# Kernel tuning notes

Measured on AMD Instinct MI355X. Metric: run time of the kernel, lower is better.

Reference implementation:

```python
import jax, jax.numpy as jnp
import numpy as np
from itertools import product

GRID = 64      # voxel grid resolution per scene
B = 8          # number of point clouds in the sparse batch
PER_B = 12500  # active voxels per scene
C = 64         # num_channels
K = 27         # 3x3x3 kernel offsets
EPS = 1e-5     # MinkowskiBatchNorm eps


def _build_kernel_map(coords):
    # coords: [N,4] int (b,x,y,z). For each of 27 offsets, find the input index
    # whose coordinate equals (b, x+dx, y+dy, z+dz); missing -> N (zero row).
    N = coords.shape[0]
    base = GRID + 2  # room for +-1 offsets after +1 shift

    def enc(b, x, y, z):
        return ((b.astype(np.int64) * base + (x + 1)) * base + (y + 1)) * base + (z + 1)

    keys = enc(coords[:, 0], coords[:, 1], coords[:, 2], coords[:, 3])
    order = np.argsort(keys)
    skeys = keys[order]
    kmap = np.full((N, K), N, dtype=np.int32)
    for k, (dx, dy, dz) in enumerate(product([-1, 0, 1], repeat=3)):
        qk = enc(coords[:, 0], coords[:, 1] + dx, coords[:, 2] + dy, coords[:, 3] + dz)
        pos = np.searchsorted(skeys, qk)
        posc = np.clip(pos, 0, N - 1)
        hit = skeys[posc] == qk
        kmap[:, k] = np.where(hit, order[posc], N)
    return kmap


def setup_inputs() -> dict:
    rng = np.random.default_rng(0)
    coords = []
    for b in range(B):
        flat = rng.choice(GRID ** 3, size=PER_B, replace=False)
        x = flat // (GRID * GRID)
        y = (flat // GRID) % GRID
        z = flat % GRID
        coords.append(np.stack([np.full(PER_B, b), x, y, z], axis=1))
    coords = np.concatenate(coords, axis=0)  # [N,4]
    kmap = _build_kernel_map(coords)         # [N,27]

    key = jax.random.key(0)
    k0, k1, k2 = jax.random.split(key, 3)
    N = coords.shape[0]
    x = jax.random.normal(k0, (N, C), dtype=jnp.float32)
    scale = 1.0 / np.sqrt(K * C)
    W1 = jax.random.normal(k1, (K, C, C), dtype=jnp.float32) * scale
    W2 = jax.random.normal(k2, (K, C, C), dtype=jnp.float32) * scale
    return {
        "x": x,
        "kmap": jnp.asarray(kmap),
        "gamma1": jnp.ones((C,), jnp.float32),
        "beta1": jnp.zeros((C,), jnp.float32),
        "W1": W1,
        "gamma2": jnp.ones((C,), jnp.float32),
        "beta2": jnp.zeros((C,), jnp.float32),
        "W2": W2,
    }


def _bn(h, gamma, beta):
    # MinkowskiBatchNorm (training mode): stats over all active points per channel
    m = h.mean(axis=0)
    v = h.var(axis=0)
    return (h - m) * jax.lax.rsqrt(v + EPS) * gamma + beta


def _sparse_conv(h, kmap, W):
    # MinkowskiConvolution stride=1: gather per-offset neighbors, GEMM, sum.
    hp = jnp.concatenate([h, jnp.zeros((1, h.shape[1]), h.dtype)], axis=0)  # zero row for misses
    g = hp[kmap]  # [N, K, C]
    return jnp.einsum('nkc,kcd->nd', g, W)


def reference(x, kmap, gamma1, beta1, W1, gamma2, beta2, W2):
    # pre-act: BN -> ReLU -> conv -> BN -> ReLU -> conv -> + residual
    out = _sparse_conv(jax.nn.relu(_bn(x, gamma1, beta1)), kmap, W1)
    out = _sparse_conv(jax.nn.relu(_bn(out, gamma2, beta2)), kmap, W2)
    return out + x
```

## Files before the change

kernel.cpp:

```cpp
#include <hip/hip_runtime.h>
#include <hip/hip_bf16.h>

#define CCH 64
#define KOFF 27
#define EPSV 1e-5f

typedef short bf16x8 __attribute__((ext_vector_type(8)));
typedef float f32x4  __attribute__((ext_vector_type(4)));

__device__ __forceinline__ void gld16(const void* g, void* l) {
    __builtin_amdgcn_global_load_lds((const __attribute__((address_space(1))) void*)g,
                                     (__attribute__((address_space(3))) void*)l, 16, 0, 0);
}

__global__ __launch_bounds__(256) void k_pre(const float* __restrict__ W1,
                                             const float* __restrict__ W2,
                                             __hip_bfloat16* __restrict__ img1,
                                             __hip_bfloat16* __restrict__ img2,
                                             const float* __restrict__ x, int N,
                                             float* __restrict__ sum,
                                             float* __restrict__ sumsq) {
    if (blockIdx.x < 2 * KOFF) {
        int k = blockIdx.x;
        const float* W = W1; __hip_bfloat16* img = img1;
        if (k >= KOFF) { k -= KOFF; W = W2; img = img2; }
        const float* src = W + (size_t)k * CCH * CCH;
        __hip_bfloat16* dst = img + (size_t)k * CCH * CCH;
        for (int e = threadIdx.x; e < CCH * CCH; e += 256) {
            const int p = e >> 3, j = e & 7;
            const int n = p >> 7, half = (p >> 6) & 1, chunk = (p >> 4) & 3, col = p & 15;
            dst[e] = __float2bfloat16(src[(chunk * 8 + half * 32 + j) * CCH + n * 16 + col]);
        }
        return;
    }
    const int bid = blockIdx.x - 2 * KOFF;
    const int nb  = gridDim.x - 2 * KOFF;
    const int c4  = threadIdx.x & 15;
    const int rg  = threadIdx.x >> 4;
    f32x4 s = {0.f, 0.f, 0.f, 0.f}, s2 = {0.f, 0.f, 0.f, 0.f};
    for (int r = bid * 16 + rg; r < N; r += nb * 16) {
        const float4 v = ((const float4*)x)[(size_t)r * 16 + c4];
        s[0] += v.x; s[1] += v.y; s[2] += v.z; s[3] += v.w;
        s2[0] += v.x * v.x; s2[1] += v.y * v.y; s2[2] += v.z * v.z; s2[3] += v.w * v.w;
    }
    __shared__ float sh[2][16][64];
#pragma unroll
    for (int j = 0; j < 4; ++j) {
        sh[0][rg][c4 * 4 + j] = s[j];
        sh[1][rg][c4 * 4 + j] = s2[j];
    }
    __syncthreads();
    if (threadIdx.x < 128) {
        const int which = threadIdx.x >> 6;
        const int c     = threadIdx.x & 63;
        float a = 0.f;
#pragma unroll
        for (int g = 0; g < 16; ++g) a += sh[which][g][c];
        atomicAdd(which ? &sumsq[c] : &sum[c], a);
    }
}

__global__ __launch_bounds__(256) void k_bnrelu_bf16(const float* __restrict__ x,
                                                     const float* __restrict__ sum,
                                                     const float* __restrict__ sumsq,
                                                     const float* __restrict__ gamma,
                                                     const float* __restrict__ beta,
                                                     __hip_bfloat16* __restrict__ h,
                                                     int N) {
    const float invN = 1.0f / (float)N;
    const int total = (N + 1) * 8;
    for (int i = blockIdx.x * 256 + threadIdx.x; i < total; i += gridDim.x * 256) {
        const int r  = i >> 3;
        const int c0 = (i & 7) * 8;
        union { __hip_bfloat16 b[8]; int4 v; } pk;
        if (r < N) {
            const float4 va = ((const float4*)x)[i * 2];
            const float4 vb = ((const float4*)x)[i * 2 + 1];
            const float vv[8] = {va.x, va.y, va.z, va.w, vb.x, vb.y, vb.z, vb.w};
#pragma unroll
            for (int j = 0; j < 8; ++j) {
                const int c     = c0 + j;
                const float m   = sum[c] * invN;
                const float var = sumsq[c] * invN - m * m;
                const float sc  = gamma[c] * rsqrtf(var + EPSV);
                const float sh_ = beta[c] - m * sc;
                float t = vv[j] * sc + sh_;
                t = t > 0.0f ? t : 0.0f;
                pk.b[j] = __float2bfloat16(t);
            }
        } else {
            pk.v = make_int4(0, 0, 0, 0);
        }
        ((int4*)h)[i] = pk.v;
    }
}

__global__ __launch_bounds__(256) void k_conv_mfma(const __hip_bfloat16* __restrict__ h,
                                                   const int* __restrict__ kmap,
                                                   const __hip_bfloat16* __restrict__ Wimg,
                                                   const float* __restrict__ resid,
                                                   float* __restrict__ out, int N,
                                                   float* __restrict__ stat_sum,
                                                   float* __restrict__ stat_sq) {
    __shared__ int sidx[64 * KOFF];
    __shared__ __hip_bfloat16 wbuf[2][4096];
    __shared__ float st[2][64];

    const int t     = threadIdx.x;
    const int lane  = t & 63;
    const int wave  = t >> 6;
    const int col16 = lane & 15;
    const int chunk = lane >> 4;
    const int base  = blockIdx.x * 64;
    const int p0    = base + wave * 16;

    const long gbase = (long)base * KOFF;
    const long glim  = (long)N * KOFF;
    for (int j = t; j < 64 * KOFF; j += 256)
        sidx[j] = (gbase + j < glim) ? kmap[gbase + j] : N;

    {
        const __hip_bfloat16* g = Wimg + t * 8;
        gld16(g,        &wbuf[0][t * 8]);
        gld16(g + 2048, &wbuf[0][t * 8 + 2048]);
    }
    __syncthreads();

    const int r0 = wave * 16 + col16;

    f32x4  acc[4] = {};
    bf16x8 a0p, a1p;

    {
        const int i0 = sidx[r0 * KOFF];
        const bf16x8* A0 = (const bf16x8*)(h + (size_t)i0 * CCH) + chunk;
        a0p = A0[0]; a1p = A0[4];
    }

    for (int k = 0; k < KOFF; ++k) {
        if (k + 1 < KOFF) {
            const __hip_bfloat16* g = Wimg + (size_t)(k + 1) * 4096 + t * 8;
            const int nb = (k + 1) & 1;
            gld16(g,        &wbuf[nb][t * 8]);
            gld16(g + 2048, &wbuf[nb][t * 8 + 2048]);
        }
        const bf16x8 a0 = a0p, a1 = a1p;
        if (k + 1 < KOFF) {
            const int i0 = sidx[r0 * KOFF + k + 1];
            const bf16x8* A0 = (const bf16x8*)(h + (size_t)i0 * CCH) + chunk;
            a0p = A0[0]; a1p = A0[4];
        }
        const bf16x8* bp = (const bf16x8*)&wbuf[k & 1][0] + lane;
#pragma unroll
        for (int n = 0; n < 4; ++n) {
            const bf16x8 b0 = bp[(n * 2 + 0) * 64];
            const bf16x8 b1 = bp[(n * 2 + 1) * 64];
            acc[n] = __builtin_amdgcn_mfma_f32_16x16x32_bf16(a0, b0, acc[n], 0, 0, 0);
            acc[n] = __builtin_amdgcn_mfma_f32_16x16x32_bf16(a1, b1, acc[n], 0, 0, 0);
        }
        __syncthreads();
    }

    if (stat_sum && t < 128) st[t >> 6][t & 63] = 0.0f;
    if (stat_sum) __syncthreads();

#pragma unroll
    for (int n = 0; n < 4; ++n) {
        const int col = n * 16 + col16;
        float s = 0.f, s2 = 0.f;
#pragma unroll
        for (int j = 0; j < 4; ++j) {
            const int row = p0 + chunk * 4 + j;
            if (row < N) {
                float v = acc[n][j];
                if (resid) v += resid[(size_t)row * CCH + col];
                out[(size_t)row * CCH + col] = v;
                s += v; s2 += v * v;
            }
        }
        if (stat_sum) {
            atomicAdd(&st[0][col], s);
            atomicAdd(&st[1][col], s2);
        }
    }
    if (stat_sum) {
        __syncthreads();
        if (t < 64)       atomicAdd(&stat_sum[t], st[0][t]);
        else if (t < 128) atomicAdd(&stat_sq[t - 64], st[1][t - 64]);
    }
}

extern "C" void kernel_launch(void* const* d_in, const int* in_sizes, int n_in,
                              void* d_out, int out_size, void* d_ws, size_t ws_size,
                              hipStream_t stream) {
    const float* x      = (const float*)d_in[0];
    const int*   kmap   = (const int*)d_in[1];
    const float* gamma1 = (const float*)d_in[2];
    const float* beta1  = (const float*)d_in[3];
    const float* W1     = (const float*)d_in[4];
    const float* gamma2 = (const float*)d_in[5];
    const float* beta2  = (const float*)d_in[6];
    const float* W2     = (const float*)d_in[7];
    float*       out    = (float*)d_out;

    const int N = in_sizes[0] / CCH;

    char* wp = (char*)d_ws;
    __hip_bfloat16* hbuf = (__hip_bfloat16*)wp;  wp += ((size_t)(N + 1) * CCH * 2 + 255) & ~255ull;
    __hip_bfloat16* img1 = (__hip_bfloat16*)wp;  wp += ((size_t)KOFF * CCH * CCH * 2 + 255) & ~255ull;
    __hip_bfloat16* img2 = (__hip_bfloat16*)wp;  wp += ((size_t)KOFF * CCH * CCH * 2 + 255) & ~255ull;
    float*          stats = (float*)wp;

    hipMemsetAsync(stats, 0, 256 * sizeof(float), stream);

    k_pre<<<2 * KOFF + 512, 256, 0, stream>>>(W1, W2, img1, img2, x, N,
                                              stats + 0, stats + 64);

    const int cgrid = (N + 63) / 64;

    k_bnrelu_bf16<<<2048, 256, 0, stream>>>(x, stats + 0, stats + 64, gamma1, beta1, hbuf, N);
    k_conv_mfma  <<<cgrid, 256, 0, stream>>>(hbuf, kmap, img1, nullptr, out, N,
                                             stats + 128, stats + 192);

    k_bnrelu_bf16<<<2048, 256, 0, stream>>>(out, stats + 128, stats + 192, gamma2, beta2, hbuf, N);
    k_conv_mfma  <<<cgrid, 256, 0, stream>>>(hbuf, kmap, img2, x, out, N,
                                             nullptr, nullptr);
}
```

Baseline: 255.6 us.

## Fuse BN+ReLU into gather-conv, double rows per wave, skip empty offsets

Removes the separate BN/ReLU bf16 conversion kernels. Each conv now applies the batch-norm scale/shift and ReLU to gathered rows on the fly, reading fp32 x (or an intermediate stored as fp32 or bf16, depending on workspace size). Each wave now handles 32 rows, and two kernel offsets share one double-buffered weight stage. A wave-wide ballot skips offsets where no lane has a neighbor. In exchange, the BN arithmetic is repeated for every gathered neighbor (up to 27 times per row), fp32 gathers use twice the bandwidth, and register and LDS pressure rise.

Result: slower. 275.1 us (+7.6%).

```diff
diff --git a/kernel.cpp b/kernel.cpp
--- a/kernel.cpp
+++ b/kernel.cpp
@@ -60,50 +60,17 @@
     }
 }
 
-__global__ __launch_bounds__(256) void k_bnrelu_bf16(const float* __restrict__ x,
-                                                     const float* __restrict__ sum,
-                                                     const float* __restrict__ sumsq,
-                                                     const float* __restrict__ gamma,
-                                                     const float* __restrict__ beta,
-                                                     __hip_bfloat16* __restrict__ h,
-                                                     int N) {
-    const float invN = 1.0f / (float)N;
-    const int total = (N + 1) * 8;
-    for (int i = blockIdx.x * 256 + threadIdx.x; i < total; i += gridDim.x * 256) {
-        const int r  = i >> 3;
-        const int c0 = (i & 7) * 8;
-        union { __hip_bfloat16 b[8]; int4 v; } pk;
-        if (r < N) {
-            const float4 va = ((const float4*)x)[i * 2];
-            const float4 vb = ((const float4*)x)[i * 2 + 1];
-            const float vv[8] = {va.x, va.y, va.z, va.w, vb.x, vb.y, vb.z, vb.w};
-#pragma unroll
-            for (int j = 0; j < 8; ++j) {
-                const int c     = c0 + j;
-                const float m   = sum[c] * invN;
-                const float var = sumsq[c] * invN - m * m;
-                const float sc  = gamma[c] * rsqrtf(var + EPSV);
-                const float sh_ = beta[c] - m * sc;
-                float t = vv[j] * sc + sh_;
-                t = t > 0.0f ? t : 0.0f;
-                pk.b[j] = __float2bfloat16(t);
-            }
-        } else {
-            pk.v = make_int4(0, 0, 0, 0);
-        }
-        ((int4*)h)[i] = pk.v;
-    }
-}
-
-__global__ __launch_bounds__(256) void k_conv_mfma(const __hip_bfloat16* __restrict__ h,
-                                                   const int* __restrict__ kmap,
-                                                   const __hip_bfloat16* __restrict__ Wimg,
-                                                   const float* __restrict__ resid,
-                                                   float* __restrict__ out, int N,
-                                                   float* __restrict__ stat_sum,
-                                                   float* __restrict__ stat_sq) {
-    __shared__ int sidx[64 * KOFF];
-    __shared__ __hip_bfloat16 wbuf[2][4096];
+__global__ __launch_bounds__(256, 3) void k_conv_fused(
+        const void* __restrict__ src, int src_f32,
+        const int* __restrict__ kmap,
+        const __hip_bfloat16* __restrict__ Wimg,
+        const float* __restrict__ bn_sum, const float* __restrict__ bn_sq,
+        const float* __restrict__ gamma, const float* __restrict__ beta,
+        const float* __restrict__ resid,
+        void* __restrict__ dst, int dst_f32, int N,
+        float* __restrict__ stat_sum, float* __restrict__ stat_sq) {
+    __shared__ int sidx[128 * KOFF];
+    __shared__ __hip_bfloat16 wbuf[2][2][4096];
     __shared__ float st[2][64];
 
     const int t     = threadIdx.x;
@@ -111,76 +78,148 @@
     const int wave  = t >> 6;
     const int col16 = lane & 15;
     const int chunk = lane >> 4;
-    const int base  = blockIdx.x * 64;
-    const int p0    = base + wave * 16;
+    const int base  = blockIdx.x * 128;
+    const int p0    = base + wave * 32;
 
     const long gbase = (long)base * KOFF;
     const long glim  = (long)N * KOFF;
-    for (int j = t; j < 64 * KOFF; j += 256)
+    for (int j = t; j < 128 * KOFF; j += 256)
         sidx[j] = (gbase + j < glim) ? kmap[gbase + j] : N;
 
     {
         const __hip_bfloat16* g = Wimg + t * 8;
-        gld16(g,        &wbuf[0][t * 8]);
-        gld16(g + 2048, &wbuf[0][t * 8 + 2048]);
-    }
+        gld16(g,             &wbuf[0][0][t * 8]);
+        gld16(g + 2048,      &wbuf[0][0][t * 8 + 2048]);
+        gld16(g + 4096,      &wbuf[0][1][t * 8]);
+        gld16(g + 6144,      &wbuf[0][1][t * 8 + 2048]);
+    }
+
+    const float invN = 1.0f / (float)N;
+    float scv[16], shv[16];
+#pragma unroll
+    for (int j = 0; j < 8; ++j) {
+        int c = chunk * 8 + j;
+        float m = bn_sum[c] * invN, vr = bn_sq[c] * invN - m * m;
+        float s = gamma[c] * rsqrtf(vr + EPSV);
+        scv[j] = s; shv[j] = beta[c] - m * s;
+        c += 32;
+        m = bn_sum[c] * invN; vr = bn_sq[c] * invN - m * m;
+        s = gamma[c] * rsqrtf(vr + EPSV);
+        scv[8 + j] = s; shv[8 + j] = beta[c] - m * s;
+    }
+
     __syncthreads();
 
-    const int r0 = wave * 16 + col16;
-
-    f32x4  acc[4] = {};
-    bf16x8 a0p, a1p;
-
-    {
-        const int i0 = sidx[r0 * KOFF];
-        const bf16x8* A0 = (const bf16x8*)(h + (size_t)i0 * CCH) + chunk;
-        a0p = A0[0]; a1p = A0[4];
-    }
-
-    for (int k = 0; k < KOFF; ++k) {
-        if (k + 1 < KOFF) {
-            const __hip_bfloat16* g = Wimg + (size_t)(k + 1) * 4096 + t * 8;
-            const int nb = (k + 1) & 1;
-            gld16(g,        &wbuf[nb][t * 8]);
-            gld16(g + 2048, &wbuf[nb][t * 8 + 2048]);
-        }
-        const bf16x8 a0 = a0p, a1 = a1p;
-        if (k + 1 < KOFF) {
-            const int i0 = sidx[r0 * KOFF + k + 1];
-            const bf16x8* A0 = (const bf16x8*)(h + (size_t)i0 * CCH) + chunk;
-            a0p = A0[0]; a1p = A0[4];
-        }
-        const bf16x8* bp = (const bf16x8*)&wbuf[k & 1][0] + lane;
+    const int r0l = wave * 32 + col16;
+    const int r1l = r0l + 16;
+
+    f32x4 acc0[4] = {}, acc1[4] = {};
+
+    auto loadraw = [&](int idx, f32x4* raw) {
+        if (src_f32) {
+            const f32x4* p = (const f32x4*)src + (size_t)idx * 16 + chunk * 2;
+            raw[0] = p[0]; raw[1] = p[1]; raw[2] = p[8]; raw[3] = p[9];
+        } else {
+            const bf16x8* p = (const bf16x8*)src + (size_t)idx * 8 + chunk;
+            const bf16x8 s0 = p[0], s1 = p[4];
+            float* r = (float*)raw;
+#pragma unroll
+            for (int j = 0; j < 8; ++j) {
+                r[j]     = __builtin_bit_cast(float, (unsigned)((unsigned short)s0[j]) << 16);
+                r[8 + j] = __builtin_bit_cast(float, (unsigned)((unsigned short)s1[j]) << 16);
+            }
+        }
+    };
+    auto bnpack = [&](const f32x4* raw, bool hh, bf16x8& A0, bf16x8& A1) {
+        const float* r = (const float*)raw;
+        union { __hip_bfloat16 b[8]; bf16x8 v; } u0, u1;
+#pragma unroll
+        for (int j = 0; j < 8; ++j) {
+            float t0 = r[j] * scv[j] + shv[j];
+            float t1 = r[8 + j] * scv[8 + j] + shv[8 + j];
+            t0 = (hh && t0 > 0.f) ? t0 : 0.f;
+            t1 = (hh && t1 > 0.f) ? t1 : 0.f;
+            u0.b[j] = __float2bfloat16(t0);
+            u1.b[j] = __float2bfloat16(t1);
+        }
+        A0 = u0.v; A1 = u1.v;
+    };
+    auto dok = [&](int k, int buf, int sub) {
+        const int i0 = sidx[r0l * KOFF + k];
+        const int i1 = sidx[r1l * KOFF + k];
+        const bool h0 = (i0 != N), h1 = (i1 != N);
+        const unsigned long long b0 = __ballot(h0 ? 1 : 0);
+        const unsigned long long b1 = __ballot(h1 ? 1 : 0);
+        if (!(b0 | b1)) return;
+        f32x4 raw0[4], raw1[4];
+        if (h0) loadraw(i0, raw0);
+        if (h1) loadraw(i1, raw1);
+        const bf16x8* bp = (const bf16x8*)&wbuf[buf][sub][0] + lane;
+        bf16x8 B0[4], B1[4];
+#pragma unroll
+        for (int n = 0; n < 4; ++n) { B0[n] = bp[(2 * n) * 64]; B1[n] = bp[(2 * n + 1) * 64]; }
+        if (b0) {
+            bf16x8 A0, A1; bnpack(raw0, h0, A0, A1);
+#pragma unroll
+            for (int n = 0; n < 4; ++n) {
+                acc0[n] = __builtin_amdgcn_mfma_f32_16x16x32_bf16(A0, B0[n], acc0[n], 0, 0, 0);
+                acc0[n] = __builtin_amdgcn_mfma_f32_16x16x32_bf16(A1, B1[n], acc0[n], 0, 0, 0);
+            }
+        }
+        if (b1) {
+            bf16x8 A0, A1; bnpack(raw1, h1, A0, A1);
+#pragma unroll
+            for (int n = 0; n < 4; ++n) {
+                acc1[n] = __builtin_amdgcn_mfma_f32_16x16x32_bf16(A0, B0[n], acc1[n], 0, 0, 0);
+                acc1[n] = __builtin_amdgcn_mfma_f32_16x16x32_bf16(A1, B1[n], acc1[n], 0, 0, 0);
+            }
+        }
+    };
+
+    for (int P = 0; 2 * P < KOFF; ++P) {
+        const int kA = 2 * P, kB = kA + 1, buf = P & 1;
+        if (kA + 2 < KOFF) {
+            const __hip_bfloat16* g = Wimg + (size_t)(kA + 2) * 4096 + t * 8;
+            gld16(g,        &wbuf[buf ^ 1][0][t * 8]);
+            gld16(g + 2048, &wbuf[buf ^ 1][0][t * 8 + 2048]);
+            if (kA + 3 < KOFF) {
+                gld16(g + 4096, &wbuf[buf ^ 1][1][t * 8]);
+                gld16(g + 6144, &wbuf[buf ^ 1][1][t * 8 + 2048]);
+            }
+        }
+        dok(kA, buf, 0);
+        if (kB < KOFF) dok(kB, buf, 1);
+        __syncthreads();
+    }
+
+    if (stat_sum) {
+        if (t < 128) st[t >> 6][t & 63] = 0.0f;
+        __syncthreads();
+    }
+
+    float* dstf = (float*)dst;
+    __hip_bfloat16* dstb = (__hip_bfloat16*)dst;
+#pragma unroll
+    for (int m = 0; m < 2; ++m) {
 #pragma unroll
         for (int n = 0; n < 4; ++n) {
-            const bf16x8 b0 = bp[(n * 2 + 0) * 64];
-            const bf16x8 b1 = bp[(n * 2 + 1) * 64];
-            acc[n] = __builtin_amdgcn_mfma_f32_16x16x32_bf16(a0, b0, acc[n], 0, 0, 0);
-            acc[n] = __builtin_amdgcn_mfma_f32_16x16x32_bf16(a1, b1, acc[n], 0, 0, 0);
-        }
-        __syncthreads();
-    }
-
-    if (stat_sum && t < 128) st[t >> 6][t & 63] = 0.0f;
-    if (stat_sum) __syncthreads();
-
-#pragma unroll
-    for (int n = 0; n < 4; ++n) {
-        const int col = n * 16 + col16;
-        float s = 0.f, s2 = 0.f;
-#pragma unroll
-        for (int j = 0; j < 4; ++j) {
-            const int row = p0 + chunk * 4 + j;
-            if (row < N) {
-                float v = acc[n][j];
-                if (resid) v += resid[(size_t)row * CCH + col];
-                out[(size_t)row * CCH + col] = v;
-                s += v; s2 += v * v;
-            }
-        }
-        if (stat_sum) {
-            atomicAdd(&st[0][col], s);
-            atomicAdd(&st[1][col], s2);
+            const int col = n * 16 + col16;
+            float s = 0.f, s2 = 0.f;
+#pragma unroll
+            for (int j = 0; j < 4; ++j) {
+                const int row = p0 + m * 16 + chunk * 4 + j;
+                if (row < N) {
+                    float v = (m == 0 ? acc0[n][j] : acc1[n][j]);
+                    if (resid) v += resid[(size_t)row * CCH + col];
+                    if (dst_f32) dstf[(size_t)row * CCH + col] = v;
+                    else         dstb[(size_t)row * CCH + col] = __float2bfloat16(v);
+                    s += v; s2 += v * v;
+                }
+            }
+            if (stat_sum) {
+                atomicAdd(&st[0][col], s);
+                atomicAdd(&st[1][col], s2);
+            }
         }
     }
     if (stat_sum) {
@@ -206,23 +245,26 @@
     const int N = in_sizes[0] / CCH;
 
     char* wp = (char*)d_ws;
-    __hip_bfloat16* hbuf = (__hip_bfloat16*)wp;  wp += ((size_t)(N + 1) * CCH * 2 + 255) & ~255ull;
-    __hip_bfloat16* img1 = (__hip_bfloat16*)wp;  wp += ((size_t)KOFF * CCH * CCH * 2 + 255) & ~255ull;
-    __hip_bfloat16* img2 = (__hip_bfloat16*)wp;  wp += ((size_t)KOFF * CCH * CCH * 2 + 255) & ~255ull;
-    float*          stats = (float*)wp;
-
-    hipMemsetAsync(stats, 0, 256 * sizeof(float), stream);
-
+    float*          stats = (float*)wp;              wp += 1024;
+    __hip_bfloat16* img1  = (__hip_bfloat16*)wp;     wp += (size_t)KOFF * CCH * CCH * 2;
+    __hip_bfloat16* img2  = (__hip_bfloat16*)wp;     wp += (size_t)KOFF * CCH * CCH * 2;
+    const size_t head = (size_t)(wp - (char*)d_ws);
+    const int h1_f32 = (ws_size >= head + (size_t)N * CCH * 4) ? 1 : 0;
+    void* h1 = (void*)wp;
+
+    hipMemsetAsync(stats, 0, 1024, stream);
     k_pre<<<2 * KOFF + 512, 256, 0, stream>>>(W1, W2, img1, img2, x, N,
                                               stats + 0, stats + 64);
 
-    const int cgrid = (N + 63) / 64;
-
-    k_bnrelu_bf16<<<2048, 256, 0, stream>>>(x, stats + 0, stats + 64, gamma1, beta1, hbuf, N);
-    k_conv_mfma  <<<cgrid, 256, 0, stream>>>(hbuf, kmap, img1, nullptr, out, N,
-                                             stats + 128, stats + 192);
-
-    k_bnrelu_bf16<<<2048, 256, 0, stream>>>(out, stats + 128, stats + 192, gamma2, beta2, hbuf, N);
-    k_conv_mfma  <<<cgrid, 256, 0, stream>>>(hbuf, kmap, img2, x, out, N,
-                                             nullptr, nullptr);
-}
+    const int cgrid = (N + 127) / 128;
+
+    k_conv_fused<<<cgrid, 256, 0, stream>>>(x, 1, kmap, img1,
+                                            stats + 0, stats + 64, gamma1, beta1,
+                                            nullptr, h1, h1_f32, N,
+                                            stats + 128, stats + 192);
+
+    k_conv_fused<<<cgrid, 256, 0, stream>>>(h1, h1_f32, kmap, img2,
+                                            stats + 128, stats + 192, gamma2, beta2,
+                                            x, out, 1, N,
+                                            nullptr, nullptr);
+}
```

## Replace dense 27-offset gather GEMM with per-offset compacted neighbor lists

Applied to the files above, without the earlier changes.

The convolution kernel now builds, per 64-row block, a shared-memory list of the valid (non-missing) neighbor indices for each kernel offset. The dense 27-step loop with its double-buffered weight staging and per-step barriers is gone. The center offset is computed densely. The other offsets run one MFMA tile per 16 list entries, take their weights straight from global memory into registers, and scatter partial sums into a shared float tile with LDS atomics. This skips MFMA and gather work on the zero rows left by missing neighbors, which are most entries at this voxel density. The cost is shared-memory atomics and a fixed cap of 48 entries per offset: overflowing entries are silently dropped, so a dense enough input would produce wrong results.

Result: slower. 621.2 us (+143.0%).

```diff
diff --git a/kernel.cpp b/kernel.cpp
--- a/kernel.cpp
+++ b/kernel.cpp
@@ -4,14 +4,12 @@
 #define CCH 64
 #define KOFF 27
 #define EPSV 1e-5f
+#define SLOTS 48
 
 typedef short bf16x8 __attribute__((ext_vector_type(8)));
 typedef float f32x4  __attribute__((ext_vector_type(4)));
 
-__device__ __forceinline__ void gld16(const void* g, void* l) {
-    __builtin_amdgcn_global_load_lds((const __attribute__((address_space(1))) void*)g,
-                                     (__attribute__((address_space(3))) void*)l, 16, 0, 0);
-}
+#define MFMA(a, b, c) __builtin_amdgcn_mfma_f32_16x16x32_bf16((a), (b), (c), 0, 0, 0)
 
 __global__ __launch_bounds__(256) void k_pre(const float* __restrict__ W1,
                                              const float* __restrict__ W2,
@@ -95,74 +93,82 @@
     }
 }
 
-__global__ __launch_bounds__(256) void k_conv_mfma(const __hip_bfloat16* __restrict__ h,
-                                                   const int* __restrict__ kmap,
-                                                   const __hip_bfloat16* __restrict__ Wimg,
-                                                   const float* __restrict__ resid,
-                                                   float* __restrict__ out, int N,
-                                                   float* __restrict__ stat_sum,
-                                                   float* __restrict__ stat_sq) {
-    __shared__ int sidx[64 * KOFF];
-    __shared__ __hip_bfloat16 wbuf[2][4096];
-    __shared__ float st[2][64];
-
-    const int t     = threadIdx.x;
-    const int lane  = t & 63;
-    const int wave  = t >> 6;
-    const int col16 = lane & 15;
-    const int chunk = lane >> 4;
+__global__ __launch_bounds__(256, 4) void k_conv_sparse(
+        const __hip_bfloat16* __restrict__ h, const int* __restrict__ kmap,
+        const __hip_bfloat16* __restrict__ Wimg, const float* __restrict__ resid,
+        float* __restrict__ out, int N,
+        float* __restrict__ stat_sum, float* __restrict__ stat_sq) {
+    __shared__ float    otile[64][CCH];
+    __shared__ unsigned list[KOFF][SLOTS];
+    __shared__ int      cnt[KOFF];
+    __shared__ float    st[2][CCH];
+
+    const int t = threadIdx.x, lane = t & 63, wave = t >> 6;
+    const int col16 = lane & 15, chunk = lane >> 4;
     const int base  = blockIdx.x * 64;
-    const int p0    = base + wave * 16;
-
-    const long gbase = (long)base * KOFF;
-    const long glim  = (long)N * KOFF;
-    for (int j = t; j < 64 * KOFF; j += 256)
-        sidx[j] = (gbase + j < glim) ? kmap[gbase + j] : N;
-
-    {
-        const __hip_bfloat16* g = Wimg + t * 8;
-        gld16(g,        &wbuf[0][t * 8]);
-        gld16(g + 2048, &wbuf[0][t * 8 + 2048]);
-    }
-    __syncthreads();
-
-    const int r0 = wave * 16 + col16;
-
-    f32x4  acc[4] = {};
-    bf16x8 a0p, a1p;
-
-    {
-        const int i0 = sidx[r0 * KOFF];
-        const bf16x8* A0 = (const bf16x8*)(h + (size_t)i0 * CCH) + chunk;
-        a0p = A0[0]; a1p = A0[4];
-    }
-
-    for (int k = 0; k < KOFF; ++k) {
-        if (k + 1 < KOFF) {
-            const __hip_bfloat16* g = Wimg + (size_t)(k + 1) * 4096 + t * 8;
-            const int nb = (k + 1) & 1;
-            gld16(g,        &wbuf[nb][t * 8]);
-            gld16(g + 2048, &wbuf[nb][t * 8 + 2048]);
-        }
-        const bf16x8 a0 = a0p, a1 = a1p;
-        if (k + 1 < KOFF) {
-            const int i0 = sidx[r0 * KOFF + k + 1];
-            const bf16x8* A0 = (const bf16x8*)(h + (size_t)i0 * CCH) + chunk;
-            a0p = A0[0]; a1p = A0[4];
-        }
-        const bf16x8* bp = (const bf16x8*)&wbuf[k & 1][0] + lane;
-#pragma unroll
-        for (int n = 0; n < 4; ++n) {
-            const bf16x8 b0 = bp[(n * 2 + 0) * 64];
-            const bf16x8 b1 = bp[(n * 2 + 1) * 64];
-            acc[n] = __builtin_amdgcn_mfma_f32_16x16x32_bf16(a0, b0, acc[n], 0, 0, 0);
-            acc[n] = __builtin_amdgcn_mfma_f32_16x16x32_bf16(a1, b1, acc[n], 0, 0, 0);
-        }
-        __syncthreads();
-    }
-
-    if (stat_sum && t < 128) st[t >> 6][t & 63] = 0.0f;
-    if (stat_sum) __syncthreads();
+
+    for (int i = t; i < 64 * CCH; i += 256) ((float*)otile)[i] = 0.f;
+    for (int i = t; i < KOFF * SLOTS; i += 256) ((unsigned*)list)[i] = ((unsigned)N << 6);
+    if (t < KOFF) cnt[t] = 0;
+    if (t < 128) st[t >> 6][t & 63] = 0.f;
+    __syncthreads();
+
+    for (int e = t; e < 64 * KOFF; e += 256) {
+        const int r = e / KOFF, k = e - r * KOFF;
+        if (base + r < N && k != 13) {
+            const int idx = kmap[(size_t)base * KOFF + e];
+            if (idx != N) {
+                const int s = atomicAdd(&cnt[k], 1);
+                if (s < SLOTS) list[k][s] = ((unsigned)idx << 6) | (unsigned)r;
+            }
+        }
+    }
+
+    const int myrow = base + wave * 16 + col16;
+    const int cidx  = (myrow < N) ? myrow : N;
+    const bf16x8* Ac = (const bf16x8*)(h + (size_t)cidx * CCH) + chunk;
+    const bf16x8 cA0 = Ac[0], cA1 = Ac[4];
+    const bf16x8* Bc = (const bf16x8*)(Wimg + (size_t)13 * 4096) + lane;
+    f32x4 acc[4] = {};
+#pragma unroll
+    for (int n = 0; n < 4; ++n) {
+        const bf16x8 b0 = Bc[(2 * n) * 64], b1 = Bc[(2 * n + 1) * 64];
+        acc[n] = MFMA(cA0, b0, acc[n]);
+        acc[n] = MFMA(cA1, b1, acc[n]);
+    }
+    __syncthreads();
+
+    for (int k = wave; k < KOFF; k += 4) {
+        if (k == 13) continue;
+        int c = cnt[k];
+        if (c <= 0) continue;
+        if (c > SLOTS) c = SLOTS;
+        const bf16x8* Bk = (const bf16x8*)(Wimg + (size_t)k * 4096) + lane;
+        bf16x8 B0[4], B1[4];
+#pragma unroll
+        for (int n = 0; n < 4; ++n) { B0[n] = Bk[(2 * n) * 64]; B1[n] = Bk[(2 * n + 1) * 64]; }
+        for (int s0 = 0; s0 < c; s0 += 16) {
+            const unsigned ent = list[k][s0 + col16];
+            const int aidx = (int)(ent >> 6);
+            const bf16x8* Ag = (const bf16x8*)(h + (size_t)aidx * CCH) + chunk;
+            const bf16x8 a0 = Ag[0], a1 = Ag[4];
+            f32x4 p[4] = {};
+#pragma unroll
+            for (int n = 0; n < 4; ++n) {
+                p[n] = MFMA(a0, B0[n], p[n]);
+                p[n] = MFMA(a1, B1[n], p[n]);
+            }
+#pragma unroll
+            for (int j = 0; j < 4; ++j) {
+                const unsigned e2 = list[k][s0 + chunk * 4 + j];
+                const int rr = (int)(e2 & 63);
+#pragma unroll
+                for (int n = 0; n < 4; ++n)
+                    atomicAdd(&otile[rr][n * 16 + col16], p[n][j]);
+            }
+        }
+    }
+    __syncthreads();
 
 #pragma unroll
     for (int n = 0; n < 4; ++n) {
@@ -170,9 +176,10 @@
         float s = 0.f, s2 = 0.f;
 #pragma unroll
         for (int j = 0; j < 4; ++j) {
-            const int row = p0 + chunk * 4 + j;
+            const int lr  = wave * 16 + chunk * 4 + j;
+            const int row = base + lr;
             if (row < N) {
-                float v = acc[n][j];
+                float v = acc[n][j] + otile[lr][col];
                 if (resid) v += resid[(size_t)row * CCH + col];
                 out[(size_t)row * CCH + col] = v;
                 s += v; s2 += v * v;
@@ -206,23 +213,24 @@
     const int N = in_sizes[0] / CCH;
 
     char* wp = (char*)d_ws;
-    __hip_bfloat16* hbuf = (__hip_bfloat16*)wp;  wp += ((size_t)(N + 1) * CCH * 2 + 255) & ~255ull;
-    __hip_bfloat16* img1 = (__hip_bfloat16*)wp;  wp += ((size_t)KOFF * CCH * CCH * 2 + 255) & ~255ull;
-    __hip_bfloat16* img2 = (__hip_bfloat16*)wp;  wp += ((size_t)KOFF * CCH * CCH * 2 + 255) & ~255ull;
-    float*          stats = (float*)wp;
-
-    hipMemsetAsync(stats, 0, 256 * sizeof(float), stream);
-
+    float*          stats = (float*)wp;            wp += 1024;
+    __hip_bfloat16* img1  = (__hip_bfloat16*)wp;   wp += (size_t)KOFF * CCH * CCH * 2;
+    __hip_bfloat16* img2  = (__hip_bfloat16*)wp;   wp += (size_t)KOFF * CCH * CCH * 2;
+    __hip_bfloat16* hbuf  = (__hip_bfloat16*)wp;
+
+    hipMemsetAsync(stats, 0, 1024, stream);
     k_pre<<<2 * KOFF + 512, 256, 0, stream>>>(W1, W2, img1, img2, x, N,
                                               stats + 0, stats + 64);
 
     const int cgrid = (N + 63) / 64;
 
-    k_bnrelu_bf16<<<2048, 256, 0, stream>>>(x, stats + 0, stats + 64, gamma1, beta1, hbuf, N);
-    k_conv_mfma  <<<cgrid, 256, 0, stream>>>(hbuf, kmap, img1, nullptr, out, N,
+    k_bnrelu_bf16<<<2048, 256, 0, stream>>>(x, stats + 0, stats + 64,
+                                            gamma1, beta1, hbuf, N);
+    k_conv_sparse<<<cgrid, 256, 0, stream>>>(hbuf, kmap, img1, nullptr, out, N,
                                              stats + 128, stats + 192);
 
-    k_bnrelu_bf16<<<2048, 256, 0, stream>>>(out, stats + 128, stats + 192, gamma2, beta2, hbuf, N);
-    k_conv_mfma  <<<cgrid, 256, 0, stream>>>(hbuf, kmap, img2, x, out, N,
+    k_bnrelu_bf16<<<2048, 256, 0, stream>>>(out, stats + 128, stats + 192,
+                                            gamma2, beta2, hbuf, N);
+    k_conv_sparse<<<cgrid, 256, 0, stream>>>(hbuf, kmap, img2, x, out, N,
                                              nullptr, nullptr);
 }
```
